# Performance work log

Measured on AMD Instinct MI355X. Metric: run time of the kernel, lower is better.

Reference implementation:

```python
import jax, jax.numpy as jnp
import numpy as np
import math

MIN_NORM = 1e-15
EPS = 1e-7
MAX_NORM = 1e6

N = 100000      # num nodes (aaa)
E = 1600000     # num edges
D_IN = 129      # embedding_num (1 time coord + 128 spatial)
D_OUT = 128     # output1_dim
MAXLEN = 50
B = 4096
NCLASS = 5

# ---------------- Hyperboloid manifold ops (HGCN-style) ----------------

def proj(x, c):
    K = 1. / c
    y = x[..., 1:]
    y_sq = jnp.sum(y * y, axis=-1, keepdims=True)
    x0 = jnp.sqrt(jnp.clip(K + y_sq, EPS))
    return jnp.concatenate([x0, y], axis=-1)

def proj_tan0(u, c):
    # zero out the time coordinate
    return jnp.concatenate([jnp.zeros_like(u[..., :1]), u[..., 1:]], axis=-1)

def expmap0(u, c):
    K = 1. / c
    sqrtK = jnp.sqrt(K)
    x = u[..., 1:]
    xn = jnp.maximum(jnp.linalg.norm(x, axis=-1, keepdims=True), MIN_NORM)
    theta = xn / sqrtK
    first = sqrtK * jnp.cosh(theta)
    rest = sqrtK * jnp.sinh(theta) * x / xn
    return proj(jnp.concatenate([first, rest], axis=-1), c)

def logmap0(x, c):
    K = 1. / c
    sqrtK = jnp.sqrt(K)
    y = x[..., 1:]
    yn = jnp.maximum(jnp.linalg.norm(y, axis=-1, keepdims=True), MIN_NORM)
    theta = jnp.clip(x[..., 0:1] / sqrtK, 1.0 + EPS)
    rest = sqrtK * jnp.arccosh(theta) * y / yn
    return jnp.concatenate([jnp.zeros_like(theta), rest], axis=-1)

def minkowski_dot(x, y):
    return jnp.sum(x * y, axis=-1, keepdims=True) - 2.0 * x[..., 0:1] * y[..., 0:1]

def minkowski_norm(u):
    return jnp.sqrt(jnp.clip(minkowski_dot(u, u), EPS))

def expmap(u, x, c):
    K = 1. / c
    sqrtK = jnp.sqrt(K)
    normu = jnp.minimum(minkowski_norm(u), MAX_NORM)
    theta = jnp.maximum(normu / sqrtK, MIN_NORM)
    result = jnp.cosh(theta) * x + jnp.sinh(theta) * u / theta
    return proj(result, c)

def proj_tan(u, x, c):
    ux = jnp.sum(x[..., 1:] * u[..., 1:], axis=-1, keepdims=True)
    vals0 = ux / jnp.clip(x[..., 0:1], EPS)
    return jnp.concatenate([vals0, u[..., 1:]], axis=-1)

def ptransp0(x, u, c):
    K = 1. / c
    sqrtK = jnp.sqrt(K)
    x0 = x[..., 0:1]
    y = x[..., 1:]
    yn = jnp.maximum(jnp.linalg.norm(y, axis=-1, keepdims=True), MIN_NORM)
    yhat = y / yn
    v = jnp.concatenate([-yn, (sqrtK - x0) * yhat], axis=-1)
    alpha = jnp.sum(yhat * u[..., 1:], axis=-1, keepdims=True) / sqrtK
    return proj_tan(u - alpha * v, x, c)

def mobius_add(x, y, c):
    u = logmap0(y, c)
    v = ptransp0(x, jnp.broadcast_to(u, x.shape), c)
    return expmap(v, x, c)

def mobius_add0(x, y, c):
    # tangent-space addition at the origin
    return expmap0(logmap0(x, c) + logmap0(y, c), c)

def mobius_matvec1(m, x, c):
    return expmap0(logmap0(x, c) @ m, c)

def mobius_matvec0(n, x, c):
    # per-row scalar mobius scaling (n is (N,1))
    return expmap0(n * logmap0(x, c), c)

def hyp_bias_point(b, c):
    return proj(expmap0(proj_tan0(b[None, :], c), c), c)

def gcn_layer(x, w, b, rows, cols, vals, c, n_nodes):
    out = mobius_matvec1(w, x, c)
    out = mobius_add(out, hyp_bias_point(b, c), c)
    out = logmap0(out, c)
    out = jax.ops.segment_sum(vals[:, None] * out[cols], rows, num_segments=n_nodes)
    return proj(expmap0(out, c), c)


def setup_inputs() -> dict:
    key = jax.random.key(0)
    ks = jax.random.split(key, 20)
    def ku(k, shape, fan_in):
        bound = 1.0 / math.sqrt(fan_in)
        return jax.random.uniform(k, shape, jnp.float32, -bound, bound)
    inp = {}
    inp['A1_tensor'] = jax.random.normal(ks[0], (N, D_IN), jnp.float32)
    inp['adj_rows'] = jax.random.randint(ks[1], (E,), 0, N)
    inp['adj_cols'] = jax.random.randint(ks[2], (E,), 0, N)
    inp['adj_vals'] = jax.random.uniform(ks[3], (E,), jnp.float32) * 0.1
    inp['batch_idx'] = jax.random.randint(ks[4], (B, 1, MAXLEN), 0, N)
    inp['raw_c'] = jnp.array([math.log(math.exp(1.0) - 1.0)], jnp.float32)
    inp['n_param'] = jax.random.uniform(ks[5], (N, 1), jnp.float32)
    inp['Lin1'] = ku(ks[6], (D_IN, D_OUT), D_IN)
    inp['Lin1_bias'] = ku(ks[7], (D_OUT,), D_IN)
    inp['gc1_w'] = ku(ks[8], (D_IN, D_OUT), D_IN)
    inp['gc1_b'] = ku(ks[9], (D_OUT,), D_IN)
    inp['gc2_w'] = ku(ks[10], (D_OUT, D_OUT), D_OUT)
    inp['gc2_b'] = ku(ks[11], (D_OUT,), D_OUT)
    inp['weight'] = ku(ks[12], (D_OUT, MAXLEN), D_OUT)
    inp['weight2'] = ku(ks[13], (D_OUT, MAXLEN), D_OUT)
    inp['conv1_w'] = ku(ks[14], (MAXLEN,), MAXLEN)
    inp['conv1_b'] = ku(ks[15], (1,), MAXLEN)
    inp['conv2_w'] = ku(ks[16], (MAXLEN,), MAXLEN)
    inp['conv2_b'] = ku(ks[17], (1,), MAXLEN)
    inp['classifier'] = ku(ks[18], (2 * MAXLEN, NCLASS), 2 * MAXLEN)
    inp['classifier_bias'] = ku(ks[19], (NCLASS,), 2 * MAXLEN)
    return inp


def reference(A1_tensor, adj_rows, adj_cols, adj_vals, batch_idx, raw_c, n_param,
              Lin1, Lin1_bias, gc1_w, gc1_b, gc2_w, gc2_b, weight, weight2,
              conv1_w, conv1_b, conv2_w, conv2_b, classifier, classifier_bias):
    c = jax.nn.softplus(raw_c)[0] + 1e-5
    bi = batch_idx[:, 0, :]                       # (B, L)
    flat = bi.reshape(-1)

    x_tan = proj_tan0(A1_tensor, c)
    a = proj(expmap0(x_tan, c), c)                # (N, D_IN)

    a1 = mobius_matvec1(Lin1, a, c)               # (N, D_OUT)
    a1 = mobius_add(a1, hyp_bias_point(Lin1_bias, c), c)
    a2 = mobius_matvec0(n_param, a1, c)

    x_1 = gcn_layer(a, gc1_w, gc1_b, adj_rows, adj_cols, adj_vals, c, N)
    x_1 = mobius_matvec0(1.0 - n_param, x_1, c)
    x_1 = mobius_add0(x_1, a2, c)
    x_2 = gcn_layer(x_1, gc2_w, gc2_b, adj_rows, adj_cols, adj_vals, c, N)

    # readout branch 1: x_2 gathered on batch indices
    s2 = logmap0(x_2[flat].reshape(bi.shape[0], bi.shape[1], D_OUT), c)  # (B,L,D)
    s2 = jnp.einsum('bld,dt->blt', s2, weight)    # (B, L, MAXLEN)
    s2 = jnp.einsum('blt,l->bt', s2, conv1_w) + conv1_b  # kernel-size-1 conv over channels

    # readout branch 2: a1 gathered on batch indices
    s3 = logmap0(a1[flat].reshape(bi.shape[0], bi.shape[1], D_OUT), c)
    s3 = jnp.einsum('bld,dt->blt', s3, weight2)
    s3 = jnp.einsum('blt,l->bt', s3, conv2_w) + conv2_b

    sel = jnp.concatenate([s2, s3], axis=1)       # (B, 2*MAXLEN)
    pre = sel @ classifier + classifier_bias      # (B, NCLASS)
    return jnp.argmax(pre, axis=-1), sel
```

## Files before the change

kernel.cpp:

```cpp
#include <hip/hip_runtime.h>
#include <math.h>


typedef unsigned short ushort_t;
typedef __attribute__((ext_vector_type(8))) short short8;
typedef __attribute__((ext_vector_type(4))) float f32x4;
typedef __attribute__((ext_vector_type(4))) unsigned short u16x4;

__device__ __forceinline__ float wsum(float x){
  x += __shfl_xor(x, 32);
  x += __shfl_xor(x, 16);
  x += __shfl_xor(x, 8);
  x += __shfl_xor(x, 4);
  x += __shfl_xor(x, 2);
  x += __shfl_xor(x, 1);
  return x;
}

__device__ __forceinline__ void get_c(const float* rc, float& K, float& sK){
  float c = log1pf(expf(rc[0])) + 1e-5f;
  K  = 1.0f / c;
  sK = sqrtf(K);
}

__device__ __forceinline__ float sinhx_over_x(float x){
  if (x > 1e-3f){
    float e  = __expf(x);
    float em = __builtin_amdgcn_rcpf(e);
    return 0.5f*(e - em) * __builtin_amdgcn_rcpf(x);
  }
  return 1.0f + x*x*(1.0f/6.0f);
}

__device__ __forceinline__ float facosh(float x){
  return __logf(x + sqrtf(fmaxf(fmaf(x, x, -1.0f), 0.0f)));
}

__device__ __forceinline__ ushort_t bf16_rne(float x){
  unsigned int u = __float_as_uint(x);
  u += 0x7fffu + ((u >> 16) & 1u);
  return (ushort_t)(u >> 16);
}
__device__ __forceinline__ float bf2f(ushort_t h){
  return __uint_as_float(((unsigned int)h) << 16);
}
__device__ __forceinline__ unsigned int pack_bf16(float x, float y){
  unsigned int bx = __float_as_uint(x);
  unsigned int by = __float_as_uint(y);
  bx = (bx + 0x7fffu + ((bx >> 16) & 1u)) >> 16;
  by = (by + 0x7fffu + ((by >> 16) & 1u)) & 0xffff0000u;
  return bx | by;
}
__device__ __forceinline__ float bf_lo(unsigned int p){ return __uint_as_float(p << 16); }
__device__ __forceinline__ float bf_hi(unsigned int p){ return __uint_as_float(p & 0xffff0000u); }

__device__ __forceinline__ void chain_scalars(float tt, float tu, float uu,
                                              float K, float sK,
                                              float& At, float& Au){
  float xn  = fmaxf(sqrtf(tt), 1e-15f);
  float th  = xn / sK;
  float f   = sinhx_over_x(th);
  float pn2 = f*f*tt;
  float p0  = sqrtf(fmaxf(K + pn2, 1e-7f));
  float S_yu = f * tu;
  float yn  = fmaxf(sqrtf(pn2), 1e-15f);
  float inv_yn = __builtin_amdgcn_rcpf(yn);
  float alpha = S_yu * inv_yn / sK;
  float coef  = alpha * (sK - p0);
  float cy  = coef * inv_yn;
  float cyf = cy * f;
  float pdw  = S_yu - cy*pn2;
  float spsq = uu - 2.f*cy*S_yu + cy*cy*pn2;
  float w0 = pdw / fmaxf(p0, 1e-7f);
  float md = spsq - w0*w0;
  float normu = fminf(sqrtf(fmaxf(md, 1e-7f)), 1e6f);
  float th2 = fmaxf(normu / sK, 1e-15f);
  float e  = __expf(th2);
  float em = __builtin_amdgcn_rcpf(e);
  float ch = 0.5f*(e + em);
  float g  = (th2 > 1e-3f) ? 0.5f*(e - em)*__builtin_amdgcn_rcpf(th2)
                           : 1.0f + th2*th2*(1.0f/6.0f);
  float rn2 = ch*ch*pn2 + 2.f*ch*g*pdw + g*g*spsq;
  float r0 = sqrtf(fmaxf(K + rn2, 1e-7f));
  float ynf = fmaxf(sqrtf(rn2), 1e-15f);
  float thf = fmaxf(r0/sK, 1.f+1e-7f);
  float rf = sK * facosh(thf) * __builtin_amdgcn_rcpf(ynf);
  At = rf*(ch*f - g*cyf);
  Au = rf*g;
}

__global__ __launch_bounds__(256) void stage_a(const float* __restrict__ A1,
                                               ushort_t* __restrict__ Lhi,
                                               ushort_t* __restrict__ Llo,
                                               int* __restrict__ cnt,
                                               const float* __restrict__ b0,
                                               const float* __restrict__ b1,
                                               const float* __restrict__ b2,
                                               float* __restrict__ uu3, int n){
  size_t i4 = (size_t)blockIdx.x * 256 + threadIdx.x;
  size_t tot4 = (size_t)n * 32;
  if (i4 < tot4){
    size_t row = i4 >> 5; int j0 = (int)(i4 & 31) * 4;
    const float* s = A1 + row*129 + 1 + j0;
    float v0 = s[0], v1 = s[1], v2 = s[2], v3 = s[3];
    ushort_t h0 = bf16_rne(v0), h1 = bf16_rne(v1), h2 = bf16_rne(v2), h3 = bf16_rne(v3);
    u16x4 hh = {h0, h1, h2, h3};
    u16x4 ll = {bf16_rne(v0 - bf2f(h0)), bf16_rne(v1 - bf2f(h1)),
                bf16_rne(v2 - bf2f(h2)), bf16_rne(v3 - bf2f(h3))};
    *(u16x4*)&Lhi[i4*4] = hh;
    *(u16x4*)&Llo[i4*4] = ll;
  }
  if (i4 < (size_t)n) cnt[i4] = 0;
  if (blockIdx.x == 0 && threadIdx.x < 64){
    int lane = threadIdx.x;
    const float* bs[3] = {b0, b1, b2};
    for (int k = 0; k < 3; ++k){
      float x = lane ? bs[k][2*lane] : 0.0f;
      float y = bs[k][2*lane+1];
      float s = wsum(x*x + y*y);
      if (lane == 0) uu3[k] = s;
    }
  }
}

__global__ __launch_bounds__(256) void split_w3(const float* __restrict__ Lin1,
                                                const float* __restrict__ G1,
                                                const float* __restrict__ G2,
                                                ushort_t* __restrict__ Wb){
  int bid = blockIdx.x;
  int which = bid >> 6, b = bid & 63;
  const float* W = (which == 0) ? (Lin1 + 128) : (which == 1) ? (G1 + 128) : G2;
  ushort_t* Whi = Wb + (size_t)which * 2 * 16384;
  ushort_t* Wlo = Whi + 16384;
  int id = b * 256 + threadIdx.x;
  int k = id >> 7, nn = id & 127;
  float v = W[(size_t)k*128 + nn];
  ushort_t h = bf16_rne(v);
  Whi[(size_t)nn*128 + k] = h;
  Wlo[(size_t)nn*128 + k] = bf16_rne(v - bf2f(h));
}

__global__ __launch_bounds__(256) void mfma_chain(const ushort_t* __restrict__ Ahi,
                                                  const ushort_t* __restrict__ Alo,
                                                  const ushort_t* __restrict__ Whi,
                                                  const ushort_t* __restrict__ Wlo,
                                                  const float* __restrict__ bias,
                                                  const float* __restrict__ uu3, int uuidx,
                                                  const float* __restrict__ raw_c,
                                                  float* __restrict__ outF,
                                                  unsigned int* __restrict__ outH,
                                                  int mode, int n, int nWaves){
  __shared__ ushort_t Wsh[2][128*128];
  int tid = threadIdx.x;
  {
    const uint4* gh = (const uint4*)Whi;
    const uint4* gl = (const uint4*)Wlo;
    uint4* sh = (uint4*)Wsh[0];
    uint4* sl = (uint4*)Wsh[1];
    #pragma unroll
    for (int i = 0; i < 8; ++i){
      int idx = tid + 256*i;
      int sw = idx ^ ((idx >> 4) & 7);
      sh[sw] = gh[idx];
    }
    #pragma unroll
    for (int i = 0; i < 8; ++i){
      int idx = tid + 256*i;
      int sw = idx ^ ((idx >> 4) & 7);
      sl[sw] = gl[idx];
    }
  }
  __syncthreads();

  int lane = tid & 63;
  int c = lane & 15, quad = lane >> 4;
  int wid = blockIdx.x * 4 + (tid >> 6);
  int nStrips = (n + 15) >> 4;
  int csw = (c & 7) << 3;

  float K, sK; get_c(raw_c, K, sK);
  float uu = uu3[uuidx];
  float uv[8];
  #pragma unroll
  for (int t = 0; t < 8; ++t){
    int col = t*16 + c;
    uv[t] = (col == 0) ? 0.f : bias[col];
  }

  for (int strip = wid; strip < nStrips; strip += nWaves){
    int m0 = strip * 16;
    int ra = m0 + c; if (ra > n - 1) ra = n - 1;
    short8 ahi[4], alo[4];
    #pragma unroll
    for (int kc = 0; kc < 4; ++kc){
      size_t aoff = (size_t)ra*128 + kc*32 + quad*8;
      ahi[kc] = *(const short8*)&Ahi[aoff];
      alo[kc] = *(const short8*)&Alo[aoff];
    }

    f32x4 acc[8];
    #pragma unroll
    for (int t = 0; t < 8; ++t){
      f32x4 z = {0.f, 0.f, 0.f, 0.f};
      acc[t] = z;
      int wrow = (t*16 + c) * 128;
      #pragma unroll
      for (int kc = 0; kc < 4; ++kc){
        int woff = (wrow + kc*32 + quad*8) ^ csw;
        short8 bhi = *(const short8*)&Wsh[0][woff];
        short8 blo = *(const short8*)&Wsh[1][woff];
        acc[t] = __builtin_amdgcn_mfma_f32_16x16x32_bf16(ahi[kc], bhi, acc[t], 0, 0, 0);
        acc[t] = __builtin_amdgcn_mfma_f32_16x16x32_bf16(ahi[kc], blo, acc[t], 0, 0, 0);
        acc[t] = __builtin_amdgcn_mfma_f32_16x16x32_bf16(alo[kc], bhi, acc[t], 0, 0, 0);
      }
    }

    if (c == 0){
      f32x4 z = {0.f, 0.f, 0.f, 0.f};
      acc[0] = z;
    }
    #pragma unroll
    for (int r = 0; r < 4; ++r){
      float tt = 0.f, tu = 0.f;
      #pragma unroll
      for (int t = 0; t < 8; ++t){
        float v = acc[t][r];
        tt = fmaf(v, v, tt);
        tu = fmaf(v, uv[t], tu);
      }
      #pragma unroll
      for (int m = 1; m <= 8; m <<= 1){
        tt += __shfl_xor(tt, m);
        tu += __shfl_xor(tu, m);
      }
      float At, Au; chain_scalars(tt, tu, uu, K, sK, At, Au);
      int row = m0 + quad*4 + r;
      if (mode == 0){
        if (row < n){
          #pragma unroll
          for (int t = 0; t < 8; ++t){
            float o = fmaf(At, acc[t][r], Au*uv[t]);
            outF[(size_t)row*128 + t*16 + c] = o;
          }
        }
      } else {
        #pragma unroll
        for (int t = 0; t < 8; ++t){
          float o  = fmaf(At, acc[t][r], Au*uv[t]);
          float on = __shfl_xor(o, 1);
          if (row < n && !(c & 1))
            outH[(size_t)row*64 + t*8 + (c >> 1)] = pack_bf16(o, on);
        }
      }
    }
  }
}

__global__ __launch_bounds__(256) void hist_k(const int* __restrict__ rows,
                                              int* __restrict__ cnt,
                                              int* __restrict__ rnk, int e){
  int base = (blockIdx.x * 256 + threadIdx.x) * 4;
  if (base + 3 < e){
    int4 r = *(const int4*)&rows[base];
    int k0 = atomicAdd(&cnt[r.x], 1);
    int k1 = atomicAdd(&cnt[r.y], 1);
    int k2 = atomicAdd(&cnt[r.z], 1);
    int k3 = atomicAdd(&cnt[r.w], 1);
    *(int4*)&rnk[base] = make_int4(k0, k1, k2, k3);
  } else {
    for (int i = base; i < e; ++i) rnk[i] = atomicAdd(&cnt[rows[i]], 1);
  }
}

#define SCAN_ITEMS 4
__global__ __launch_bounds__(256) void scan1(const int* __restrict__ cnt,
                                             int* __restrict__ off,
                                             int* __restrict__ bsum, int n){
  __shared__ int sh[256];
  int tid = threadIdx.x;
  int base = blockIdx.x * 256 * SCAN_ITEMS + tid * SCAN_ITEMS;
  int v[SCAN_ITEMS]; int s = 0;
  #pragma unroll
  for (int i = 0; i < SCAN_ITEMS; ++i){ int idx = base+i; v[i] = (idx < n) ? cnt[idx] : 0; s += v[i]; }
  sh[tid] = s; __syncthreads();
  for (int o = 1; o < 256; o <<= 1){
    int t = (tid >= o) ? sh[tid - o] : 0; __syncthreads();
    sh[tid] += t; __syncthreads();
  }
  int excl = sh[tid] - s;
  if (tid == 255) bsum[blockIdx.x] = sh[tid];
  int run = excl;
  #pragma unroll
  for (int i = 0; i < SCAN_ITEMS; ++i){ int idx = base+i; if (idx < n) off[idx] = run; run += v[i]; }
}

__global__ __launch_bounds__(256) void scan2(int* __restrict__ bsum, int G){
  __shared__ int sh[256];
  int t = threadIdx.x;
  int v = (t < G) ? bsum[t] : 0;
  sh[t] = v; __syncthreads();
  for (int o = 1; o < 256; o <<= 1){
    int x = (t >= o) ? sh[t - o] : 0; __syncthreads();
    sh[t] += x; __syncthreads();
  }
  if (t < G) bsum[t] = sh[t] - v;
}

__global__ void scan3(int* __restrict__ off, const int* __restrict__ bsum, int n){
  int i = blockIdx.x * blockDim.x + threadIdx.x;
  if (i < n) off[i] += bsum[i / (256*SCAN_ITEMS)];
}

__global__ __launch_bounds__(256) void fill_k(const int* __restrict__ rows,
                                              const int* __restrict__ cols,
                                              const float* __restrict__ vals,
                                              const int* __restrict__ off,
                                              const int* __restrict__ rnk,
                                              int2* __restrict__ ecv, int e){
  int base = (blockIdx.x * 256 + threadIdx.x) * 4;
  if (base + 3 < e){
    int4   r = *(const int4*)&rows[base];
    int4   q = *(const int4*)&rnk[base];
    int4   c = *(const int4*)&cols[base];
    float4 v = *(const float4*)&vals[base];
    int o0 = off[r.x], o1 = off[r.y], o2 = off[r.z], o3 = off[r.w];
    ecv[o0 + q.x] = make_int2(c.x, __float_as_int(v.x));
    ecv[o1 + q.y] = make_int2(c.y, __float_as_int(v.y));
    ecv[o2 + q.z] = make_int2(c.z, __float_as_int(v.z));
    ecv[o3 + q.w] = make_int2(c.w, __float_as_int(v.w));
  } else {
    for (int i = base; i < e; ++i)
      ecv[off[rows[i]] + rnk[i]] = make_int2(cols[i], __float_as_int(vals[i]));
  }
}

__device__ __forceinline__ float2 seg_gather_bf16(const unsigned int* __restrict__ h,
                                                  const int* __restrict__ off,
                                                  const int* __restrict__ cnt,
                                                  const int2* __restrict__ ecv,
                                                  int row, int lane){
  float ax = 0.f, ay = 0.f, bx = 0.f, by = 0.f;
  int st = off[row], deg = cnt[row];
  const unsigned int* __restrict__ hb = h + lane;
  for (int b = 0; b < deg; b += 64){
    int k = b + lane;
    int cc = 0; float vv = 0.f;
    if (k < deg){ int2 e = ecv[st+k]; cc = e.x; vv = __int_as_float(e.y); }
    int m = min(64, deg - b);
    for (int j = 0; j < m; j += 8){
      int   c0=__shfl(cc,j+0), c1=__shfl(cc,j+1), c2=__shfl(cc,j+2), c3=__shfl(cc,j+3);
      int   c4=__shfl(cc,j+4), c5=__shfl(cc,j+5), c6=__shfl(cc,j+6), c7=__shfl(cc,j+7);
      float v0=__shfl(vv,j+0), v1=__shfl(vv,j+1), v2=__shfl(vv,j+2), v3=__shfl(vv,j+3);
      float v4=__shfl(vv,j+4), v5=__shfl(vv,j+5), v6=__shfl(vv,j+6), v7=__shfl(vv,j+7);
      unsigned int p0 = hb[(size_t)c0*64];
      unsigned int p1 = hb[(size_t)c1*64];
      unsigned int p2 = hb[(size_t)c2*64];
      unsigned int p3 = hb[(size_t)c3*64];
      unsigned int p4 = hb[(size_t)c4*64];
      unsigned int p5 = hb[(size_t)c5*64];
      unsigned int p6 = hb[(size_t)c6*64];
      unsigned int p7 = hb[(size_t)c7*64];
      ax = fmaf(v0, bf_lo(p0), ax); ay = fmaf(v0, bf_hi(p0), ay);
      bx = fmaf(v1, bf_lo(p1), bx); by = fmaf(v1, bf_hi(p1), by);
      ax = fmaf(v2, bf_lo(p2), ax); ay = fmaf(v2, bf_hi(p2), ay);
      bx = fmaf(v3, bf_lo(p3), bx); by = fmaf(v3, bf_hi(p3), by);
      ax = fmaf(v4, bf_lo(p4), ax); ay = fmaf(v4, bf_hi(p4), ay);
      bx = fmaf(v5, bf_lo(p5), bx); by = fmaf(v5, bf_hi(p5), by);
      ax = fmaf(v6, bf_lo(p6), ax); ay = fmaf(v6, bf_hi(p6), ay);
      bx = fmaf(v7, bf_lo(p7), bx); by = fmaf(v7, bf_hi(p7), by);
    }
  }
  return make_float2(ax + bx, ay + by);
}

__global__ __launch_bounds__(256) void seg_x1(const unsigned int* __restrict__ h1,
                                              const int* __restrict__ off,
                                              const int* __restrict__ cnt,
                                              const int2* __restrict__ ecv,
                                              const float* __restrict__ loga1,
                                              const float* __restrict__ nparam,
                                              unsigned int* __restrict__ X1hi,
                                              unsigned int* __restrict__ X1lo, int n){
  int row  = (int)((blockIdx.x * blockDim.x + threadIdx.x) >> 6);
  int lane = threadIdx.x & 63;
  if (row >= n) return;
  float2 acc = seg_gather_bf16(h1, off, cnt, ecv, row, lane);
  float nv = nparam[row];
  float2 la1 = *(const float2*)&loga1[(size_t)row*128 + 2*lane];
  float ox = (1.f-nv)*acc.x + nv*la1.x;
  float oy = (1.f-nv)*acc.y + nv*la1.y;
  unsigned int hp = pack_bf16(ox, oy);
  X1hi[(size_t)row*64 + lane] = hp;
  X1lo[(size_t)row*64 + lane] = pack_bf16(ox - bf_lo(hp), oy - bf_hi(hp));
}

__global__ __launch_bounds__(256) void seg_x2(const unsigned int* __restrict__ h2,
                                              const int* __restrict__ off,
                                              const int* __restrict__ cnt,
                                              const int2* __restrict__ ecv,
                                              unsigned int* __restrict__ Lx2p, int n){
  int row  = (int)((blockIdx.x * blockDim.x + threadIdx.x) >> 6);
  int lane = threadIdx.x & 63;
  if (row >= n) return;
  float2 acc = seg_gather_bf16(h2, off, cnt, ecv, row, lane);
  Lx2p[(size_t)row*64 + lane] = pack_bf16(acc.x, acc.y);
}

__global__ __launch_bounds__(128) void batch_head(const unsigned int* __restrict__ Lx2p,
                                                  const float* __restrict__ loga1,
                                                  const int* __restrict__ bidx,
                                                  const float* __restrict__ weight,
                                                  const float* __restrict__ weight2,
                                                  const float* __restrict__ c1w,
                                                  const float* __restrict__ c1b,
                                                  const float* __restrict__ c2w,
                                                  const float* __restrict__ c2b,
                                                  const float* __restrict__ cls,
                                                  const float* __restrict__ clsb,
                                                  float* __restrict__ out, int Bn){
  __shared__ float sg2[128], sg3[128], ssel[100], spre[5];
  __shared__ int sbi[50];
  __shared__ float sc1[50], sc2[50];
  int b = blockIdx.x, d = threadIdx.x;
  const int* bi = bidx + (size_t)b * 50;
  if (d < 50){ sbi[d] = bi[d]; sc1[d] = c1w[d]; sc2[d] = c2w[d]; }
  __syncthreads();
  int lane = d & 63;
  bool lo = d < 64;
  float gx = 0.f, gy = 0.f;
  if (lo){
    const unsigned int* __restrict__ tp = Lx2p + lane;
    #pragma unroll
    for (int l = 0; l < 50; l += 5){
      int i0 = sbi[l+0], i1 = sbi[l+1], i2 = sbi[l+2], i3 = sbi[l+3], i4 = sbi[l+4];
      unsigned int p0 = tp[(size_t)i0*64];
      unsigned int p1 = tp[(size_t)i1*64];
      unsigned int p2 = tp[(size_t)i2*64];
      unsigned int p3 = tp[(size_t)i3*64];
      unsigned int p4 = tp[(size_t)i4*64];
      float w0 = sc1[l+0], w1 = sc1[l+1], w2 = sc1[l+2], w3 = sc1[l+3], w4 = sc1[l+4];
      gx = fmaf(w0, bf_lo(p0), gx); gy = fmaf(w0, bf_hi(p0), gy);
      gx = fmaf(w1, bf_lo(p1), gx); gy = fmaf(w1, bf_hi(p1), gy);
      gx = fmaf(w2, bf_lo(p2), gx); gy = fmaf(w2, bf_hi(p2), gy);
      gx = fmaf(w3, bf_lo(p3), gx); gy = fmaf(w3, bf_hi(p3), gy);
      gx = fmaf(w4, bf_lo(p4), gx); gy = fmaf(w4, bf_hi(p4), gy);
    }
    sg2[2*lane] = gx; sg2[2*lane+1] = gy;
  } else {
    const float2* __restrict__ t2 = (const float2*)loga1 + lane;
    #pragma unroll
    for (int l = 0; l < 50; l += 5){
      int i0 = sbi[l+0], i1 = sbi[l+1], i2 = sbi[l+2], i3 = sbi[l+3], i4 = sbi[l+4];
      float2 p0 = t2[(size_t)i0*64];
      float2 p1 = t2[(size_t)i1*64];
      float2 p2 = t2[(size_t)i2*64];
      float2 p3 = t2[(size_t)i3*64];
      float2 p4 = t2[(size_t)i4*64];
      float w0 = sc2[l+0], w1 = sc2[l+1], w2 = sc2[l+2], w3 = sc2[l+3], w4 = sc2[l+4];
      gx = fmaf(w0, p0.x, gx); gy = fmaf(w0, p0.y, gy);
      gx = fmaf(w1, p1.x, gx); gy = fmaf(w1, p1.y, gy);
      gx = fmaf(w2, p2.x, gx); gy = fmaf(w2, p2.y, gy);
      gx = fmaf(w3, p3.x, gx); gy = fmaf(w3, p3.y, gy);
      gx = fmaf(w4, p4.x, gx); gy = fmaf(w4, p4.y, gy);
    }
    sg3[2*lane] = gx; sg3[2*lane+1] = gy;
  }
  __syncthreads();
  if (d < 50){
    float s = 0.f;
    for (int k = 0; k < 128; ++k) s = fmaf(sg2[k], weight[k*50 + d], s);
    s += c1b[0];
    ssel[d] = s;
    out[(size_t)Bn + (size_t)b*100 + d] = s;
  } else if (d >= 64 && d < 114){
    int t = d - 64;
    float s = 0.f;
    for (int k = 0; k < 128; ++k) s = fmaf(sg3[k], weight2[k*50 + t], s);
    s += c2b[0];
    ssel[50 + t] = s;
    out[(size_t)Bn + (size_t)b*100 + 50 + t] = s;
  }
  __syncthreads();
  if (d < 5){
    float s = clsb[d];
    for (int j = 0; j < 100; ++j) s = fmaf(ssel[j], cls[j*5 + d], s);
    spre[d] = s;
  }
  __syncthreads();
  if (d == 0){
    int best = 0; float bv = spre[0];
    #pragma unroll
    for (int k = 1; k < 5; ++k) if (spre[k] > bv){ bv = spre[k]; best = k; }
    out[b] = (float)best;
  }
}

extern "C" void kernel_launch(void* const* d_in, const int* in_sizes, int n_in,
                              void* d_out, int out_size, void* d_ws, size_t ws_size,
                              hipStream_t stream) {
  const float* A1     = (const float*)d_in[0];
  const int*   rows   = (const int*)  d_in[1];
  const int*   cols   = (const int*)  d_in[2];
  const float* vals   = (const float*)d_in[3];
  const int*   bidx   = (const int*)  d_in[4];
  const float* raw_c  = (const float*)d_in[5];
  const float* nparam = (const float*)d_in[6];
  const float* Lin1   = (const float*)d_in[7];
  const float* Lin1_b = (const float*)d_in[8];
  const float* gc1_w  = (const float*)d_in[9];
  const float* gc1_b  = (const float*)d_in[10];
  const float* gc2_w  = (const float*)d_in[11];
  const float* gc2_b  = (const float*)d_in[12];
  const float* weight = (const float*)d_in[13];
  const float* weight2= (const float*)d_in[14];
  const float* c1w    = (const float*)d_in[15];
  const float* c1b    = (const float*)d_in[16];
  const float* c2w    = (const float*)d_in[17];
  const float* c2b    = (const float*)d_in[18];
  const float* cls    = (const float*)d_in[19];
  const float* clsb   = (const float*)d_in[20];

  int N  = in_sizes[0] / 129;
  int E  = in_sizes[1];
  int Bn = in_sizes[4] / 50;
  size_t NF = (size_t)N * 128;

  ushort_t* Lhi = (ushort_t*)d_ws;
  ushort_t* Llo = Lhi + NF;
  unsigned int* Lx2p = (unsigned int*)d_ws;
  float*    S3  = (float*)(Llo + NF);
  unsigned int* Hb   = (unsigned int*)(S3 + NF);
  unsigned int* X1hi = Hb + NF/2;
  unsigned int* X1lo = X1hi + NF/2;
  ushort_t* Wb = (ushort_t*)(X1lo + NF/2);
  ushort_t* W1h = Wb,           *W1l = Wb + 16384;
  ushort_t* W2h = Wb + 2*16384, *W2l = Wb + 3*16384;
  ushort_t* W3h = Wb + 4*16384, *W3l = Wb + 5*16384;
  int* cnt    = (int*)(Wb + 6*16384);
  int* off    = cnt + N;
  int* rnk    = off + N;
  int* bsum   = rnk + E;
  int2* ecv   = (int2*)(bsum + 4096);
  float* uu3  = (float*)(ecv + E);

  int rowBlocks  = (N + 3) / 4;
  int G = (N + 256*SCAN_ITEMS - 1) / (256*SCAN_ITEMS);
  int eBlocks4 = (E/4 + 255) / 256 + 1;
  int mBlocks = 512;
  int nWaves  = mBlocks * 4;

  stage_a<<<(int)(((size_t)N*32 + 255)/256), 256, 0, stream>>>(A1, Lhi, Llo, cnt,
                                                     Lin1_b, gc1_b, gc2_b, uu3, N);
  split_w3<<<192, 256, 0, stream>>>(Lin1, gc1_w, gc2_w, Wb);

  hist_k<<<eBlocks4, 256, 0, stream>>>(rows, cnt, rnk, E);
  scan1<<<G, 256, 0, stream>>>(cnt, off, bsum, N);
  scan2<<<1, 256, 0, stream>>>(bsum, G);
  scan3<<<(N+255)/256, 256, 0, stream>>>(off, bsum, N);
  fill_k<<<eBlocks4, 256, 0, stream>>>(rows, cols, vals, off, rnk, ecv, E);

  mfma_chain<<<mBlocks, 256, 0, stream>>>(Lhi, Llo, W1h, W1l, Lin1_b, uu3, 0, raw_c,
                                          S3, (unsigned int*)nullptr, 0, N, nWaves);
  mfma_chain<<<mBlocks, 256, 0, stream>>>(Lhi, Llo, W2h, W2l, gc1_b, uu3, 1, raw_c,
                                          (float*)nullptr, Hb, 1, N, nWaves);
  seg_x1<<<rowBlocks, 256, 0, stream>>>(Hb, off, cnt, ecv, S3, nparam, X1hi, X1lo, N);
  mfma_chain<<<mBlocks, 256, 0, stream>>>((const ushort_t*)X1hi, (const ushort_t*)X1lo,
                                          W3h, W3l, gc2_b, uu3, 2, raw_c,
                                          (float*)nullptr, Hb, 1, N, nWaves);
  seg_x2<<<rowBlocks, 256, 0, stream>>>(Hb, off, cnt, ecv, Lx2p, N);
  batch_head<<<Bn, 128, 0, stream>>>(Lx2p, S3, bidx, weight, weight2, c1w, c1b,
                                     c2w, c2b, cls, clsb, (float*)d_out, Bn);
}
```

Measured before the change: 576.3 us.

## Fuse bf16 split into dual-weight MFMA kernel and drop scan3 pass

Removes the stage_a pre-pass that split A1 into hi/lo bf16 arrays; a new mfma_dual kernel reads fp32 A1 directly, splits it in registers, and computes both the Lin1 and gc1 matmul chains in one pass with all four weight halves held in 128 KB of LDS. It also folds the scan3 block-offset add into consumers by adding bsum[row>>10] on the fly, and moves the cnt zeroing and bias-norm setup into split_w3. This removes two full-size intermediate arrays and a second read of A1, at the cost of heavy LDS use (one block per CU), more registers for two accumulator sets, and an extra bsum load in the fill and gather kernels.

```diff
diff --git a/kernel.cpp b/kernel.cpp
--- a/kernel.cpp
+++ b/kernel.cpp
@@ -5,7 +5,6 @@
 typedef unsigned short ushort_t;
 typedef __attribute__((ext_vector_type(8))) short short8;
 typedef __attribute__((ext_vector_type(4))) float f32x4;
-typedef __attribute__((ext_vector_type(4))) unsigned short u16x4;
 
 __device__ __forceinline__ float wsum(float x){
   x += __shfl_xor(x, 32);
@@ -89,44 +88,15 @@
   Au = rf*g;
 }
 
-__global__ __launch_bounds__(256) void stage_a(const float* __restrict__ A1,
-                                               ushort_t* __restrict__ Lhi,
-                                               ushort_t* __restrict__ Llo,
-                                               int* __restrict__ cnt,
-                                               const float* __restrict__ b0,
-                                               const float* __restrict__ b1,
-                                               const float* __restrict__ b2,
-                                               float* __restrict__ uu3, int n){
-  size_t i4 = (size_t)blockIdx.x * 256 + threadIdx.x;
-  size_t tot4 = (size_t)n * 32;
-  if (i4 < tot4){
-    size_t row = i4 >> 5; int j0 = (int)(i4 & 31) * 4;
-    const float* s = A1 + row*129 + 1 + j0;
-    float v0 = s[0], v1 = s[1], v2 = s[2], v3 = s[3];
-    ushort_t h0 = bf16_rne(v0), h1 = bf16_rne(v1), h2 = bf16_rne(v2), h3 = bf16_rne(v3);
-    u16x4 hh = {h0, h1, h2, h3};
-    u16x4 ll = {bf16_rne(v0 - bf2f(h0)), bf16_rne(v1 - bf2f(h1)),
-                bf16_rne(v2 - bf2f(h2)), bf16_rne(v3 - bf2f(h3))};
-    *(u16x4*)&Lhi[i4*4] = hh;
-    *(u16x4*)&Llo[i4*4] = ll;
-  }
-  if (i4 < (size_t)n) cnt[i4] = 0;
-  if (blockIdx.x == 0 && threadIdx.x < 64){
-    int lane = threadIdx.x;
-    const float* bs[3] = {b0, b1, b2};
-    for (int k = 0; k < 3; ++k){
-      float x = lane ? bs[k][2*lane] : 0.0f;
-      float y = bs[k][2*lane+1];
-      float s = wsum(x*x + y*y);
-      if (lane == 0) uu3[k] = s;
-    }
-  }
-}
-
 __global__ __launch_bounds__(256) void split_w3(const float* __restrict__ Lin1,
                                                 const float* __restrict__ G1,
                                                 const float* __restrict__ G2,
-                                                ushort_t* __restrict__ Wb){
+                                                ushort_t* __restrict__ Wb,
+                                                const float* __restrict__ b0,
+                                                const float* __restrict__ b1,
+                                                const float* __restrict__ b2,
+                                                float* __restrict__ uu3,
+                                                int* __restrict__ cnt, int n){
   int bid = blockIdx.x;
   int which = bid >> 6, b = bid & 63;
   const float* W = (which == 0) ? (Lin1 + 128) : (which == 1) ? (G1 + 128) : G2;
@@ -138,6 +108,151 @@
   ushort_t h = bf16_rne(v);
   Whi[(size_t)nn*128 + k] = h;
   Wlo[(size_t)nn*128 + k] = bf16_rne(v - bf2f(h));
+  for (int i = bid*256 + threadIdx.x; i < n; i += 192*256) cnt[i] = 0;
+  if (bid == 0 && threadIdx.x < 64){
+    int lane = threadIdx.x;
+    const float* bs[3] = {b0, b1, b2};
+    for (int kk = 0; kk < 3; ++kk){
+      float x = lane ? bs[kk][2*lane] : 0.0f;
+      float y = bs[kk][2*lane+1];
+      float s = wsum(x*x + y*y);
+      if (lane == 0) uu3[kk] = s;
+    }
+  }
+}
+
+__global__ __launch_bounds__(512) void mfma_dual(const float* __restrict__ A1f,
+                                                 const ushort_t* __restrict__ W1hi,
+                                                 const ushort_t* __restrict__ W1lo,
+                                                 const ushort_t* __restrict__ W2hi,
+                                                 const ushort_t* __restrict__ W2lo,
+                                                 const float* __restrict__ bias1,
+                                                 const float* __restrict__ bias2,
+                                                 const float* __restrict__ uu3,
+                                                 const float* __restrict__ raw_c,
+                                                 float* __restrict__ outF,
+                                                 unsigned int* __restrict__ outH,
+                                                 int n, int nWaves){
+  __shared__ ushort_t Wsh[4][128*128];
+  int tid = threadIdx.x;
+  {
+    const uint4* g0 = (const uint4*)W1hi;
+    const uint4* g1 = (const uint4*)W1lo;
+    const uint4* g2 = (const uint4*)W2hi;
+    const uint4* g3 = (const uint4*)W2lo;
+    uint4* s0 = (uint4*)Wsh[0]; uint4* s1 = (uint4*)Wsh[1];
+    uint4* s2 = (uint4*)Wsh[2]; uint4* s3 = (uint4*)Wsh[3];
+    #pragma unroll
+    for (int i = 0; i < 4; ++i){
+      int idx = tid + 512*i;
+      int sw = idx ^ ((idx >> 4) & 7);
+      s0[sw] = g0[idx];
+      s1[sw] = g1[idx];
+      s2[sw] = g2[idx];
+      s3[sw] = g3[idx];
+    }
+  }
+  __syncthreads();
+
+  int lane = tid & 63;
+  int c = lane & 15, quad = lane >> 4;
+  int wid = blockIdx.x * 8 + (tid >> 6);
+  int nStrips = (n + 15) >> 4;
+  int csw = (c & 7) << 3;
+
+  float K, sK; get_c(raw_c, K, sK);
+  float uu1 = uu3[0], uu2 = uu3[1];
+  float uv1[8], uv2[8];
+  #pragma unroll
+  for (int t = 0; t < 8; ++t){
+    int col = t*16 + c;
+    uv1[t] = (col == 0) ? 0.f : bias1[col];
+    uv2[t] = (col == 0) ? 0.f : bias2[col];
+  }
+
+  for (int strip = wid; strip < nStrips; strip += nWaves){
+    int m0 = strip * 16;
+    int ra = m0 + c; if (ra > n - 1) ra = n - 1;
+    short8 ahi[4], alo[4];
+    {
+      const float* ap = A1f + (size_t)ra*129 + 1;
+      #pragma unroll
+      for (int kc = 0; kc < 4; ++kc){
+        int aoff = kc*32 + quad*8;
+        #pragma unroll
+        for (int j = 0; j < 8; ++j){
+          float v = ap[aoff + j];
+          ushort_t h = bf16_rne(v);
+          ahi[kc][j] = (short)h;
+          alo[kc][j] = (short)bf16_rne(v - bf2f(h));
+        }
+      }
+    }
+
+    f32x4 acc1[8], acc2[8];
+    #pragma unroll
+    for (int t = 0; t < 8; ++t){
+      f32x4 z = {0.f, 0.f, 0.f, 0.f};
+      acc1[t] = z; acc2[t] = z;
+      int wrow = (t*16 + c) * 128;
+      #pragma unroll
+      for (int kc = 0; kc < 4; ++kc){
+        int woff = (wrow + kc*32 + quad*8) ^ csw;
+        short8 b1h = *(const short8*)&Wsh[0][woff];
+        short8 b1l = *(const short8*)&Wsh[1][woff];
+        short8 b2h = *(const short8*)&Wsh[2][woff];
+        short8 b2l = *(const short8*)&Wsh[3][woff];
+        acc1[t] = __builtin_amdgcn_mfma_f32_16x16x32_bf16(ahi[kc], b1h, acc1[t], 0, 0, 0);
+        acc1[t] = __builtin_amdgcn_mfma_f32_16x16x32_bf16(ahi[kc], b1l, acc1[t], 0, 0, 0);
+        acc1[t] = __builtin_amdgcn_mfma_f32_16x16x32_bf16(alo[kc], b1h, acc1[t], 0, 0, 0);
+        acc2[t] = __builtin_amdgcn_mfma_f32_16x16x32_bf16(ahi[kc], b2h, acc2[t], 0, 0, 0);
+        acc2[t] = __builtin_amdgcn_mfma_f32_16x16x32_bf16(ahi[kc], b2l, acc2[t], 0, 0, 0);
+        acc2[t] = __builtin_amdgcn_mfma_f32_16x16x32_bf16(alo[kc], b2h, acc2[t], 0, 0, 0);
+      }
+    }
+
+    if (c == 0){
+      f32x4 z = {0.f, 0.f, 0.f, 0.f};
+      acc1[0] = z; acc2[0] = z;
+    }
+    #pragma unroll
+    for (int r = 0; r < 4; ++r){
+      float tt1 = 0.f, tu1 = 0.f, tt2 = 0.f, tu2 = 0.f;
+      #pragma unroll
+      for (int t = 0; t < 8; ++t){
+        float v1 = acc1[t][r];
+        tt1 = fmaf(v1, v1, tt1);
+        tu1 = fmaf(v1, uv1[t], tu1);
+        float v2 = acc2[t][r];
+        tt2 = fmaf(v2, v2, tt2);
+        tu2 = fmaf(v2, uv2[t], tu2);
+      }
+      #pragma unroll
+      for (int m = 1; m <= 8; m <<= 1){
+        tt1 += __shfl_xor(tt1, m);
+        tu1 += __shfl_xor(tu1, m);
+        tt2 += __shfl_xor(tt2, m);
+        tu2 += __shfl_xor(tu2, m);
+      }
+      float At1, Au1; chain_scalars(tt1, tu1, uu1, K, sK, At1, Au1);
+      float At2, Au2; chain_scalars(tt2, tu2, uu2, K, sK, At2, Au2);
+      int row = m0 + quad*4 + r;
+      if (row < n){
+        #pragma unroll
+        for (int t = 0; t < 8; ++t){
+          float o = fmaf(At1, acc1[t][r], Au1*uv1[t]);
+          outF[(size_t)row*128 + t*16 + c] = o;
+        }
+      }
+      #pragma unroll
+      for (int t = 0; t < 8; ++t){
+        float o  = fmaf(At2, acc2[t][r], Au2*uv2[t]);
+        float on = __shfl_xor(o, 1);
+        if (row < n && !(c & 1))
+          outH[(size_t)row*64 + t*8 + (c >> 1)] = pack_bf16(o, on);
+      }
+    }
+  }
 }
 
 __global__ __launch_bounds__(256) void mfma_chain(const ushort_t* __restrict__ Ahi,
@@ -147,9 +262,8 @@
                                                   const float* __restrict__ bias,
                                                   const float* __restrict__ uu3, int uuidx,
                                                   const float* __restrict__ raw_c,
-                                                  float* __restrict__ outF,
                                                   unsigned int* __restrict__ outH,
-                                                  int mode, int n, int nWaves){
+                                                  int n, int nWaves){
   __shared__ ushort_t Wsh[2][128*128];
   int tid = threadIdx.x;
   {
@@ -235,22 +349,12 @@
       }
       float At, Au; chain_scalars(tt, tu, uu, K, sK, At, Au);
       int row = m0 + quad*4 + r;
-      if (mode == 0){
-        if (row < n){
-          #pragma unroll
-          for (int t = 0; t < 8; ++t){
-            float o = fmaf(At, acc[t][r], Au*uv[t]);
-            outF[(size_t)row*128 + t*16 + c] = o;
-          }
-        }
-      } else {
-        #pragma unroll
-        for (int t = 0; t < 8; ++t){
-          float o  = fmaf(At, acc[t][r], Au*uv[t]);
-          float on = __shfl_xor(o, 1);
-          if (row < n && !(c & 1))
-            outH[(size_t)row*64 + t*8 + (c >> 1)] = pack_bf16(o, on);
-        }
+      #pragma unroll
+      for (int t = 0; t < 8; ++t){
+        float o  = fmaf(At, acc[t][r], Au*uv[t]);
+        float on = __shfl_xor(o, 1);
+        if (row < n && !(c & 1))
+          outH[(size_t)row*64 + t*8 + (c >> 1)] = pack_bf16(o, on);
       }
     }
   }
@@ -306,15 +410,11 @@
   if (t < G) bsum[t] = sh[t] - v;
 }
 
-__global__ void scan3(int* __restrict__ off, const int* __restrict__ bsum, int n){
-  int i = blockIdx.x * blockDim.x + threadIdx.x;
-  if (i < n) off[i] += bsum[i / (256*SCAN_ITEMS)];
-}
-
 __global__ __launch_bounds__(256) void fill_k(const int* __restrict__ rows,
                                               const int* __restrict__ cols,
                                               const float* __restrict__ vals,
                                               const int* __restrict__ off,
+                                              const int* __restrict__ bsum,
                                               const int* __restrict__ rnk,
                                               int2* __restrict__ ecv, int e){
   int base = (blockIdx.x * 256 + threadIdx.x) * 4;
@@ -323,24 +423,28 @@
     int4   q = *(const int4*)&rnk[base];
     int4   c = *(const int4*)&cols[base];
     float4 v = *(const float4*)&vals[base];
-    int o0 = off[r.x], o1 = off[r.y], o2 = off[r.z], o3 = off[r.w];
+    int o0 = off[r.x] + bsum[r.x >> 10];
+    int o1 = off[r.y] + bsum[r.y >> 10];
+    int o2 = off[r.z] + bsum[r.z >> 10];
+    int o3 = off[r.w] + bsum[r.w >> 10];
     ecv[o0 + q.x] = make_int2(c.x, __float_as_int(v.x));
     ecv[o1 + q.y] = make_int2(c.y, __float_as_int(v.y));
     ecv[o2 + q.z] = make_int2(c.z, __float_as_int(v.z));
     ecv[o3 + q.w] = make_int2(c.w, __float_as_int(v.w));
   } else {
     for (int i = base; i < e; ++i)
-      ecv[off[rows[i]] + rnk[i]] = make_int2(cols[i], __float_as_int(vals[i]));
+      ecv[off[rows[i]] + bsum[rows[i] >> 10] + rnk[i]] = make_int2(cols[i], __float_as_int(vals[i]));
   }
 }
 
 __device__ __forceinline__ float2 seg_gather_bf16(const unsigned int* __restrict__ h,
                                                   const int* __restrict__ off,
+                                                  const int* __restrict__ bsum,
                                                   const int* __restrict__ cnt,
                                                   const int2* __restrict__ ecv,
                                                   int row, int lane){
   float ax = 0.f, ay = 0.f, bx = 0.f, by = 0.f;
-  int st = off[row], deg = cnt[row];
+  int st = off[row] + bsum[row >> 10], deg = cnt[row];
   const unsigned int* __restrict__ hb = h + lane;
   for (int b = 0; b < deg; b += 64){
     int k = b + lane;
@@ -375,6 +479,7 @@
 
 __global__ __launch_bounds__(256) void seg_x1(const unsigned int* __restrict__ h1,
                                               const int* __restrict__ off,
+                                              const int* __restrict__ bsum,
                                               const int* __restrict__ cnt,
                                               const int2* __restrict__ ecv,
                                               const float* __restrict__ loga1,
@@ -384,7 +489,7 @@
   int row  = (int)((blockIdx.x * blockDim.x + threadIdx.x) >> 6);
   int lane = threadIdx.x & 63;
   if (row >= n) return;
-  float2 acc = seg_gather_bf16(h1, off, cnt, ecv, row, lane);
+  float2 acc = seg_gather_bf16(h1, off, bsum, cnt, ecv, row, lane);
   float nv = nparam[row];
   float2 la1 = *(const float2*)&loga1[(size_t)row*128 + 2*lane];
   float ox = (1.f-nv)*acc.x + nv*la1.x;
@@ -396,13 +501,14 @@
 
 __global__ __launch_bounds__(256) void seg_x2(const unsigned int* __restrict__ h2,
                                               const int* __restrict__ off,
+                                              const int* __restrict__ bsum,
                                               const int* __restrict__ cnt,
                                               const int2* __restrict__ ecv,
                                               unsigned int* __restrict__ Lx2p, int n){
   int row  = (int)((blockIdx.x * blockDim.x + threadIdx.x) >> 6);
   int lane = threadIdx.x & 63;
   if (row >= n) return;
-  float2 acc = seg_gather_bf16(h2, off, cnt, ecv, row, lane);
+  float2 acc = seg_gather_bf16(h2, off, bsum, cnt, ecv, row, lane);
   Lx2p[(size_t)row*64 + lane] = pack_bf16(acc.x, acc.y);
 }
 
@@ -525,10 +631,8 @@
   int Bn = in_sizes[4] / 50;
   size_t NF = (size_t)N * 128;
 
-  ushort_t* Lhi = (ushort_t*)d_ws;
-  ushort_t* Llo = Lhi + NF;
   unsigned int* Lx2p = (unsigned int*)d_ws;
-  float*    S3  = (float*)(Llo + NF);
+  float*    S3  = (float*)((char*)d_ws + 4*NF);
   unsigned int* Hb   = (unsigned int*)(S3 + NF);
   unsigned int* X1hi = Hb + NF/2;
   unsigned int* X1lo = X1hi + NF/2;
@@ -546,28 +650,24 @@
   int rowBlocks  = (N + 3) / 4;
   int G = (N + 256*SCAN_ITEMS - 1) / (256*SCAN_ITEMS);
   int eBlocks4 = (E/4 + 255) / 256 + 1;
-  int mBlocks = 512;
-  int nWaves  = mBlocks * 4;
-
-  stage_a<<<(int)(((size_t)N*32 + 255)/256), 256, 0, stream>>>(A1, Lhi, Llo, cnt,
-                                                     Lin1_b, gc1_b, gc2_b, uu3, N);
-  split_w3<<<192, 256, 0, stream>>>(Lin1, gc1_w, gc2_w, Wb);
+
+  split_w3<<<192, 256, 0, stream>>>(Lin1, gc1_w, gc2_w, Wb,
+                                    Lin1_b, gc1_b, gc2_b, uu3, cnt, N);
 
   hist_k<<<eBlocks4, 256, 0, stream>>>(rows, cnt, rnk, E);
   scan1<<<G, 256, 0, stream>>>(cnt, off, bsum, N);
   scan2<<<1, 256, 0, stream>>>(bsum, G);
-  scan3<<<(N+255)/256, 256, 0, stream>>>(off, bsum, N);
-  fill_k<<<eBlocks4, 256, 0, stream>>>(rows, cols, vals, off, rnk, ecv, E);
-
-  mfma_chain<<<mBlocks, 256, 0, stream>>>(Lhi, Llo, W1h, W1l, Lin1_b, uu3, 0, raw_c,
-                                          S3, (unsigned int*)nullptr, 0, N, nWaves);
-  mfma_chain<<<mBlocks, 256, 0, stream>>>(Lhi, Llo, W2h, W2l, gc1_b, uu3, 1, raw_c,
-                                          (float*)nullptr, Hb, 1, N, nWaves);
-  seg_x1<<<rowBlocks, 256, 0, stream>>>(Hb, off, cnt, ecv, S3, nparam, X1hi, X1lo, N);
-  mfma_chain<<<mBlocks, 256, 0, stream>>>((const ushort_t*)X1hi, (const ushort_t*)X1lo,
-                                          W3h, W3l, gc2_b, uu3, 2, raw_c,
-                                          (float*)nullptr, Hb, 1, N, nWaves);
-  seg_x2<<<rowBlocks, 256, 0, stream>>>(Hb, off, cnt, ecv, Lx2p, N);
+  fill_k<<<eBlocks4, 256, 0, stream>>>(rows, cols, vals, off, bsum, rnk, ecv, E);
+
+  mfma_dual<<<256, 512, 0, stream>>>(A1, W1h, W1l, W2h, W2l,
+                                     Lin1_b, gc1_b, uu3, raw_c,
+                                     S3, Hb, N, 256*8);
+  seg_x1<<<rowBlocks, 256, 0, stream>>>(Hb, off, bsum, cnt, ecv, S3, nparam,
+                                        X1hi, X1lo, N);
+  mfma_chain<<<512, 256, 0, stream>>>((const ushort_t*)X1hi, (const ushort_t*)X1lo,
+                                      W3h, W3l, gc2_b, uu3, 2, raw_c,
+                                      Hb, N, 512*4);
+  seg_x2<<<rowBlocks, 256, 0, stream>>>(Hb, off, bsum, cnt, ecv, Lx2p, N);
   batch_head<<<Bn, 128, 0, stream>>>(Lx2p, S3, bidx, weight, weight2, c1w, c1b,
                                      c2w, c2b, cls, clsb, (float*)d_out, Bn);
 }
```

Measured after the change: 746.6 us. 29.6% more time.
